# Performance work log

Measured on AMD Instinct MI355X. Metric: run time of the kernel, lower is better.

The kernel has to match this reference:

```python
import jax, jax.numpy as jnp
import numpy as np

B, N, C, H = 4, 1024, 1024, 16
HD = C // H


def setup_inputs() -> dict:
    key = jax.random.key(0)
    ks = jax.random.split(key, 9)
    s = 0.02
    return {
        "x": jax.random.normal(ks[0], (B, N, C), dtype=jnp.float32),
        "qkv_w": jax.random.normal(ks[1], (3 * C, C), dtype=jnp.float32) * s,
        "qkv_b": jax.random.normal(ks[2], (3 * C,), dtype=jnp.float32) * s,
        "proj_w": jax.random.normal(ks[3], (C, C), dtype=jnp.float32) * s,
        "proj_b": jax.random.normal(ks[4], (C,), dtype=jnp.float32) * s,
        "wl": jax.random.normal(ks[5], (H, H), dtype=jnp.float32) * s,
        "bl": jax.random.normal(ks[6], (H,), dtype=jnp.float32) * s,
        "ww": jax.random.normal(ks[7], (H, H), dtype=jnp.float32) * s,
        "bw": jax.random.normal(ks[8], (H,), dtype=jnp.float32) * s,
    }


def reference(x, qkv_w, qkv_b, proj_w, proj_b, wl, bl, ww, bw):
    # qkv: torch Linear convention y = x @ W.T + b
    scale = HD ** (-0.5)
    qkv = (jnp.einsum("bnc,oc->bno", x, qkv_w) + qkv_b)
    qkv = qkv.reshape(B, N, 3, H, HD).transpose(2, 0, 3, 1, 4)  # [3,B,H,N,HD]
    q, k, v = qkv[0] * scale, qkv[1], qkv[2]
    attn = jnp.einsum("bhnd,bhmd->bhnm", q, k)  # [B,H,N,N]
    # talking-heads mix before softmax (proj_l over head dim)
    attn = jnp.einsum("bhnm,gh->bgnm", attn, wl) + bl[:, None, None]
    attn = jax.nn.softmax(attn, axis=-1)
    # talking-heads mix after softmax (proj_w over head dim)
    attn = jnp.einsum("bhnm,gh->bgnm", attn, ww) + bw[:, None, None]
    out = jnp.einsum("bhnm,bhmd->bhnd", attn, v)  # [B,H,N,HD]
    out = out.transpose(0, 2, 1, 3).reshape(B, N, C)
    out = jnp.einsum("bnc,oc->bno", out, proj_w) + proj_b
    return out, attn
```

## Files before the change

kernel.cpp:

```cpp
#include <hip/hip_runtime.h>
#include <hip/hip_bf16.h>

typedef unsigned short u16;
typedef __attribute__((ext_vector_type(8))) __bf16 bf16x8;
typedef __attribute__((ext_vector_type(4))) float f32x4;

template <typename T> struct is16 { static constexpr bool v = false; };
template <> struct is16<u16> { static constexpr bool v = true; };

__device__ __forceinline__ float bf2f(u16 u) {
    unsigned int x = ((unsigned int)u) << 16;
    return __builtin_bit_cast(float, x);
}
__device__ __forceinline__ u16 f2bf(float f) {
    unsigned int x = __builtin_bit_cast(unsigned int, f);
    unsigned int lsb = (x >> 16) & 1u;
    x += 0x7fffu + lsb;
    return (u16)(x >> 16);
}

__device__ __forceinline__ void ld8(u16* dst, const u16* src) {
    *(float4*)dst = *(const float4*)src;
}
__device__ __forceinline__ void ld8(u16* dst, const float* src) {
    float4 a = *(const float4*)src;
    float4 b = *(const float4*)(src + 4);
    u16 t[8];
    t[0] = f2bf(a.x); t[1] = f2bf(a.y); t[2] = f2bf(a.z); t[3] = f2bf(a.w);
    t[4] = f2bf(b.x); t[5] = f2bf(b.y); t[6] = f2bf(b.z); t[7] = f2bf(b.w);
    *(float4*)dst = *(float4*)t;
}
__device__ __forceinline__ void stC(u16* p, float v)   { *p = f2bf(v); }
__device__ __forceinline__ void stC(float* p, float v) { *p = v; }

__device__ __forceinline__ void g2l16(const void* g, void* l) {
    __builtin_amdgcn_global_load_lds(
        (const __attribute__((address_space(1))) void*)g,
        (__attribute__((address_space(3))) void*)l, 16, 0, 0);
}

__global__ __launch_bounds__(256)
void cvt_bf16(const float* __restrict__ src, u16* __restrict__ dst)
{
    long long t = blockIdx.x * 256 + threadIdx.x;
    u16 tmp[8];
    ld8(tmp, src + t * 8);
    *(float4*)(dst + t * 8) = *(float4*)tmp;
}

template <typename TA, typename TB, typename TC>
__global__ __launch_bounds__(256)
void gemm_nt(const TA* __restrict__ A, long long sA, int lda,
             const TB* __restrict__ B, long long sB, int ldb,
             TC* __restrict__ C, long long sC, int ldc,
             const float* __restrict__ bias, int K)
{
    constexpr int SA = is16<TA>::v ? 32 : 40;
    constexpr int SB = is16<TB>::v ? 32 : 40;
    __shared__ u16 As[128 * SA];
    __shared__ u16 Bs[128 * SB];

    const int tid = threadIdx.x;
    const int z = blockIdx.z;
    A += (long long)z * sA;
    B += (long long)z * sB;
    C += (long long)z * sC;
    const int m0 = blockIdx.y * 128;
    const int n0 = blockIdx.x * 128;
    const int wid = tid >> 6;
    const int lane = tid & 63;
    const int wm = (wid >> 1) * 64;
    const int wn = (wid & 1) * 64;
    const int lr = lane & 15;
    const int quad = lane >> 4;

    f32x4 acc[4][4];
#pragma unroll
    for (int i = 0; i < 4; i++)
#pragma unroll
        for (int j = 0; j < 4; j++)
#pragma unroll
            for (int r = 0; r < 4; r++) acc[i][j][r] = 0.f;

    const int srow = tid >> 2;
    const int scol = (tid & 3) * 8;

    for (int k0 = 0; k0 < K; k0 += 32) {
        __syncthreads();
        const TA* ga = A + (long long)(m0 + srow) * lda + k0 + scol;
        if constexpr (is16<TA>::v) {
            g2l16(ga, (char*)As + tid * 16);
            g2l16(ga + (long long)64 * lda, (char*)As + 4096 + tid * 16);
        } else {
            ld8(&As[srow * SA + scol], ga);
            ld8(&As[(srow + 64) * SA + scol], ga + (long long)64 * lda);
        }
        const TB* gb = B + (long long)(n0 + srow) * ldb + k0 + scol;
        if constexpr (is16<TB>::v) {
            g2l16(gb, (char*)Bs + tid * 16);
            g2l16(gb + (long long)64 * ldb, (char*)Bs + 4096 + tid * 16);
        } else {
            ld8(&Bs[srow * SB + scol], gb);
            ld8(&Bs[(srow + 64) * SB + scol], gb + (long long)64 * ldb);
        }
        __syncthreads();

        bf16x8 af[4], bfr[4];
#pragma unroll
        for (int t = 0; t < 4; t++) {
            af[t]  = *(const bf16x8*)&As[(wm + t * 16 + lr) * SA + quad * 8];
            bfr[t] = *(const bf16x8*)&Bs[(wn + t * 16 + lr) * SB + quad * 8];
        }
#pragma unroll
        for (int i = 0; i < 4; i++)
#pragma unroll
            for (int j = 0; j < 4; j++)
                acc[i][j] = __builtin_amdgcn_mfma_f32_16x16x32_bf16(af[i], bfr[j], acc[i][j], 0, 0, 0);
    }

#pragma unroll
    for (int j = 0; j < 4; j++) {
        const int col = n0 + wn + j * 16 + lr;
        const float bv = bias ? bias[col] : 0.f;
#pragma unroll
        for (int i = 0; i < 4; i++) {
            const int rbase = m0 + wm + i * 16 + quad * 4;
#pragma unroll
            for (int r = 0; r < 4; r++)
                stC(&C[(long long)(rbase + r) * ldc + col], acc[i][j][r] + bv);
        }
    }
}

__global__ __launch_bounds__(256)
void reorder_qkv(const u16* __restrict__ y, u16* __restrict__ q,
                 u16* __restrict__ k, u16* __restrict__ v)
{
    int t = blockIdx.x * 256 + threadIdx.x;
    int which = t >> 19;
    int r = t & 524287;
    int d8 = r & 7;
    int n = (r >> 3) & 1023;
    int h = (r >> 13) & 15;
    int b = r >> 17;
    const u16* src = y + ((long long)(b * 1024 + n)) * 3072 + which * 1024 + h * 64 + d8 * 8;
    u16* dst = (which == 0 ? q : (which == 1 ? k : v)) +
               (((long long)((b * 16 + h) * 1024 + n)) * 64 + d8 * 8);
    float4 val = *(const float4*)src;
    if (which == 0) {
        u16 tmp[8];
        *(float4*)tmp = val;
#pragma unroll
        for (int i = 0; i < 8; i++) tmp[i] = f2bf(bf2f(tmp[i]) * 0.125f);
        val = *(float4*)tmp;
    }
    *(float4*)dst = val;
}

__global__ __launch_bounds__(256)
void mix_softmax(const u16* __restrict__ S, float* __restrict__ attn_out,
                 u16* __restrict__ attn_bf,
                 const float* __restrict__ wl, const float* __restrict__ bl,
                 const float* __restrict__ ww, const float* __restrict__ bw)
{
    __shared__ float wlT[256];
    __shared__ float wwS[256];
    __shared__ float blS[16];
    __shared__ float bwS[16];
    __shared__ float red[64];
    __shared__ float gsum[16];

    const int tid = threadIdx.x;
    const int lane = tid & 63;
    const int wid = tid >> 6;
    const int b = blockIdx.x >> 10, n = blockIdx.x & 1023;
    const int m0 = tid * 4;

    const long long base = ((long long)(b * 16) * 1024 + n) * 1024 + m0;

    ushort4 pre[4];
#pragma unroll
    for (int h = 0; h < 4; h++)
        pre[h] = *(const ushort4*)(S + base + (long long)h * 1048576);

    wlT[(tid & 15) * 16 + (tid >> 4)] = wl[tid];
    if (tid < 16) { blS[tid] = bl[tid]; bwS[tid] = bw[tid]; }
    __syncthreads();

    f32x4 a[16];
#pragma unroll
    for (int g = 0; g < 16; g++) {
        float bv = blS[g];
        a[g] = (f32x4){bv, bv, bv, bv};
    }

#pragma unroll
    for (int h = 0; h < 16; h++) {
        ushort4 r = pre[h & 3];
        if (h + 4 < 16)
            pre[h & 3] = *(const ushort4*)(S + base + (long long)(h + 4) * 1048576);
        f32x4 sv;
        sv.x = bf2f(r.x); sv.y = bf2f(r.y); sv.z = bf2f(r.z); sv.w = bf2f(r.w);
        float wr[16];
        *(f32x4*)&wr[0]  = *(const f32x4*)&wlT[h * 16];
        *(f32x4*)&wr[4]  = *(const f32x4*)&wlT[h * 16 + 4];
        *(f32x4*)&wr[8]  = *(const f32x4*)&wlT[h * 16 + 8];
        *(f32x4*)&wr[12] = *(const f32x4*)&wlT[h * 16 + 12];
#pragma unroll
        for (int g = 0; g < 16; g++)
            a[g] += sv * wr[g];
    }

#pragma unroll
    for (int g = 0; g < 16; g++) {
        f32x4 p;
        p.x = __expf(a[g].x);
        p.y = __expf(a[g].y);
        p.z = __expf(a[g].z);
        p.w = __expf(a[g].w);
        a[g] = p;
        float vv = (p.x + p.y) + (p.z + p.w);
        for (int off = 32; off; off >>= 1) vv += __shfl_xor(vv, off, 64);
        if (lane == 0) red[wid * 16 + g] = vv;
    }
    __syncthreads();
    if (tid < 16)
        gsum[tid] = (red[tid] + red[16 + tid]) + (red[32 + tid] + red[48 + tid]);
    __syncthreads();
    wwS[tid] = ww[tid] / gsum[tid & 15];
    __syncthreads();

#pragma unroll
    for (int g = 0; g < 16; g++) {
        float wr[16];
        *(f32x4*)&wr[0]  = *(const f32x4*)&wwS[g * 16];
        *(f32x4*)&wr[4]  = *(const f32x4*)&wwS[g * 16 + 4];
        *(f32x4*)&wr[8]  = *(const f32x4*)&wwS[g * 16 + 8];
        *(f32x4*)&wr[12] = *(const f32x4*)&wwS[g * 16 + 12];
        float bv = bwS[g];
        f32x4 o = (f32x4){bv, bv, bv, bv};
#pragma unroll
        for (int h = 0; h < 16; h++)
            o += a[h] * wr[h];
        const long long off = base + (long long)g * 1048576;
        __builtin_nontemporal_store(o, (f32x4*)(attn_out + off));
        ushort4 bo;
        bo.x = f2bf(o.x); bo.y = f2bf(o.y); bo.z = f2bf(o.z); bo.w = f2bf(o.w);
        *(ushort4*)(attn_bf + off) = bo;
    }
}

__global__ __launch_bounds__(256)
void av_gemm(const u16* __restrict__ attn_bf, const u16* __restrict__ v,
             u16* __restrict__ out1)
{
    __shared__ u16 As[64 * 32];
    __shared__ u16 Bs[64 * 40];

    const int tid = threadIdx.x;
    const int z = blockIdx.z;
    const int b = z >> 4, h = z & 15;
    const int m0 = blockIdx.x * 64;
    const u16* Ab = attn_bf + (long long)z * 1048576;
    const u16* Vb = v + (long long)z * 65536;
    const int wid = tid >> 6;
    const int lane = tid & 63;
    const int lr = lane & 15;
    const int quad = lane >> 4;
    const int wm = wid * 16;

    f32x4 acc[4];
#pragma unroll
    for (int j = 0; j < 4; j++)
#pragma unroll
        for (int r = 0; r < 4; r++) acc[j][r] = 0.f;

    const int srow = tid >> 2;
    const int scol = (tid & 3) * 8;
    const int vrow = tid >> 3;
    const int vdb = (tid & 7) * 8;

    for (int k0 = 0; k0 < 1024; k0 += 32) {
        __syncthreads();
        g2l16(Ab + (long long)(m0 + srow) * 1024 + k0 + scol, (char*)As + tid * 16);
        u16 tmp[8];
        *(float4*)tmp = *(const float4*)(Vb + (long long)(k0 + vrow) * 64 + vdb);
#pragma unroll
        for (int j = 0; j < 8; j++) Bs[(vdb + j) * 40 + vrow] = tmp[j];
        __syncthreads();

        bf16x8 af, bfr[4];
        af = *(const bf16x8*)&As[(wm + lr) * 32 + quad * 8];
#pragma unroll
        for (int t = 0; t < 4; t++)
            bfr[t] = *(const bf16x8*)&Bs[(t * 16 + lr) * 40 + quad * 8];
#pragma unroll
        for (int j = 0; j < 4; j++)
            acc[j] = __builtin_amdgcn_mfma_f32_16x16x32_bf16(af, bfr[j], acc[j], 0, 0, 0);
    }

#pragma unroll
    for (int j = 0; j < 4; j++) {
        const int col = h * 64 + j * 16 + lr;
        const int rbase = m0 + wm + quad * 4;
#pragma unroll
        for (int r = 0; r < 4; r++)
            out1[(long long)(b * 1024 + rbase + r) * 1024 + col] = f2bf(acc[j][r]);
    }
}

extern "C" void kernel_launch(void* const* d_in, const int* in_sizes, int n_in,
                              void* d_out, int out_size, void* d_ws, size_t ws_size,
                              hipStream_t stream)
{
    const float* x      = (const float*)d_in[0];
    const float* qkv_w  = (const float*)d_in[1];
    const float* qkv_b  = (const float*)d_in[2];
    const float* proj_w = (const float*)d_in[3];
    const float* proj_b = (const float*)d_in[4];
    const float* wl     = (const float*)d_in[5];
    const float* bl     = (const float*)d_in[6];
    const float* ww     = (const float*)d_in[7];
    const float* bw     = (const float*)d_in[8];

    float* out      = (float*)d_out;
    float* attn_out = out + 4194304;

    u16* ws   = (u16*)d_ws;
    u16* y    = ws;
    u16* q    = ws + 12582912;
    u16* k    = ws + 16777216;
    u16* v    = ws + 20971520;
    u16* s    = ws + 25165824;
    u16* out1 = ws;

    u16* xb  = s;
    u16* qwb = s + 4194304;
    u16* pwb = q;

    dim3 blk(256);
    cvt_bf16<<<dim3(2048), blk, 0, stream>>>(x, xb);
    cvt_bf16<<<dim3(1536), blk, 0, stream>>>(qkv_w, qwb);
    gemm_nt<u16, u16, u16><<<dim3(24, 32, 1), blk, 0, stream>>>(
        xb, 0, 1024, qwb, 0, 1024, y, 0, 3072, qkv_b, 1024);
    reorder_qkv<<<dim3(6144), blk, 0, stream>>>(y, q, k, v);
    gemm_nt<u16, u16, u16><<<dim3(8, 8, 64), blk, 0, stream>>>(
        q, 65536, 64, k, 65536, 64, s, 1048576, 1024, nullptr, 64);
    cvt_bf16<<<dim3(512), blk, 0, stream>>>(proj_w, pwb);
    mix_softmax<<<dim3(4096), blk, 0, stream>>>(s, attn_out, s, wl, bl, ww, bw);
    av_gemm<<<dim3(16, 1, 64), blk, 0, stream>>>(s, v, out1);
    gemm_nt<u16, u16, float><<<dim3(8, 32, 1), blk, 0, stream>>>(
        out1, 0, 1024, pwb, 0, 1024, out, 0, 1024, proj_b, 1024);
}
```

Baseline: 608.9 us.

## Remove QKV reorder kernel by strided GEMM reads and fuse bf16 conversions

```diff
diff --git a/kernel.cpp b/kernel.cpp
--- a/kernel.cpp
+++ b/kernel.cpp
@@ -40,20 +40,27 @@
 }
 
 __global__ __launch_bounds__(256)
-void cvt_bf16(const float* __restrict__ src, u16* __restrict__ dst)
-{
-    long long t = blockIdx.x * 256 + threadIdx.x;
+void cvt_all(const float* __restrict__ x, const float* __restrict__ qw,
+             const float* __restrict__ pw, u16* __restrict__ xb,
+             u16* __restrict__ qwb, u16* __restrict__ pwb)
+{
+    long long t = (long long)blockIdx.x * 256 + threadIdx.x;
+    const float* src; u16* dst; long long o;
+    if (t < 524288)      { src = x;  dst = xb;  o = t; }
+    else if (t < 917504) { src = qw; dst = qwb; o = t - 524288; }
+    else                 { src = pw; dst = pwb; o = t - 917504; }
     u16 tmp[8];
-    ld8(tmp, src + t * 8);
-    *(float4*)(dst + t * 8) = *(float4*)tmp;
+    ld8(tmp, src + o * 8);
+    *(float4*)(dst + o * 8) = *(float4*)tmp;
 }
 
 template <typename TA, typename TB, typename TC>
 __global__ __launch_bounds__(256)
-void gemm_nt(const TA* __restrict__ A, long long sA, int lda,
-             const TB* __restrict__ B, long long sB, int ldb,
-             TC* __restrict__ C, long long sC, int ldc,
-             const float* __restrict__ bias, int K)
+void gemm_nt(const TA* __restrict__ A, long long sAb, long long sAh, int lda,
+             const TB* __restrict__ B, long long sBb, long long sBh, int ldb,
+             TC* __restrict__ C, long long sCb, long long sCh, int ldc,
+             const float* __restrict__ bias, int K, int zdiv,
+             float cscale, int csplit)
 {
     constexpr int SA = is16<TA>::v ? 32 : 40;
     constexpr int SB = is16<TB>::v ? 32 : 40;
@@ -62,9 +69,10 @@
 
     const int tid = threadIdx.x;
     const int z = blockIdx.z;
-    A += (long long)z * sA;
-    B += (long long)z * sB;
-    C += (long long)z * sC;
+    const int zb = z / zdiv, zh = z % zdiv;
+    A += zb * sAb + zh * sAh;
+    B += zb * sBb + zh * sBh;
+    C += zb * sCb + zh * sCh;
     const int m0 = blockIdx.y * 128;
     const int n0 = blockIdx.x * 128;
     const int wid = tid >> 6;
@@ -122,39 +130,15 @@
     for (int j = 0; j < 4; j++) {
         const int col = n0 + wn + j * 16 + lr;
         const float bv = bias ? bias[col] : 0.f;
+        const float scl = (col < csplit) ? cscale : 1.f;
 #pragma unroll
         for (int i = 0; i < 4; i++) {
             const int rbase = m0 + wm + i * 16 + quad * 4;
 #pragma unroll
             for (int r = 0; r < 4; r++)
-                stC(&C[(long long)(rbase + r) * ldc + col], acc[i][j][r] + bv);
+                stC(&C[(long long)(rbase + r) * ldc + col], (acc[i][j][r] + bv) * scl);
         }
     }
-}
-
-__global__ __launch_bounds__(256)
-void reorder_qkv(const u16* __restrict__ y, u16* __restrict__ q,
-                 u16* __restrict__ k, u16* __restrict__ v)
-{
-    int t = blockIdx.x * 256 + threadIdx.x;
-    int which = t >> 19;
-    int r = t & 524287;
-    int d8 = r & 7;
-    int n = (r >> 3) & 1023;
-    int h = (r >> 13) & 15;
-    int b = r >> 17;
-    const u16* src = y + ((long long)(b * 1024 + n)) * 3072 + which * 1024 + h * 64 + d8 * 8;
-    u16* dst = (which == 0 ? q : (which == 1 ? k : v)) +
-               (((long long)((b * 16 + h) * 1024 + n)) * 64 + d8 * 8);
-    float4 val = *(const float4*)src;
-    if (which == 0) {
-        u16 tmp[8];
-        *(float4*)tmp = val;
-#pragma unroll
-        for (int i = 0; i < 8; i++) tmp[i] = f2bf(bf2f(tmp[i]) * 0.125f);
-        val = *(float4*)tmp;
-    }
-    *(float4*)dst = val;
 }
 
 __global__ __launch_bounds__(256)
@@ -178,9 +162,9 @@
 
     const long long base = ((long long)(b * 16) * 1024 + n) * 1024 + m0;
 
-    ushort4 pre[4];
-#pragma unroll
-    for (int h = 0; h < 4; h++)
+    ushort4 pre[8];
+#pragma unroll
+    for (int h = 0; h < 8; h++)
         pre[h] = *(const ushort4*)(S + base + (long long)h * 1048576);
 
     wlT[(tid & 15) * 16 + (tid >> 4)] = wl[tid];
@@ -196,9 +180,9 @@
 
 #pragma unroll
     for (int h = 0; h < 16; h++) {
-        ushort4 r = pre[h & 3];
-        if (h + 4 < 16)
-            pre[h & 3] = *(const ushort4*)(S + base + (long long)(h + 4) * 1048576);
+        ushort4 r = pre[h & 7];
+        if (h + 8 < 16)
+            pre[h & 7] = *(const ushort4*)(S + base + (long long)(h + 8) * 1048576);
         f32x4 sv;
         sv.x = bf2f(r.x); sv.y = bf2f(r.y); sv.z = bf2f(r.z); sv.w = bf2f(r.w);
         float wr[16];
@@ -251,7 +235,7 @@
 }
 
 __global__ __launch_bounds__(256)
-void av_gemm(const u16* __restrict__ attn_bf, const u16* __restrict__ v,
+void av_gemm(const u16* __restrict__ attn_bf, const u16* __restrict__ y,
              u16* __restrict__ out1)
 {
     __shared__ u16 As[64 * 32];
@@ -262,7 +246,7 @@
     const int b = z >> 4, h = z & 15;
     const int m0 = blockIdx.x * 64;
     const u16* Ab = attn_bf + (long long)z * 1048576;
-    const u16* Vb = v + (long long)z * 65536;
+    const u16* Vb = y + (long long)b * 3145728 + 2048 + h * 64;
     const int wid = tid >> 6;
     const int lane = tid & 63;
     const int lr = lane & 15;
@@ -284,7 +268,7 @@
         __syncthreads();
         g2l16(Ab + (long long)(m0 + srow) * 1024 + k0 + scol, (char*)As + tid * 16);
         u16 tmp[8];
-        *(float4*)tmp = *(const float4*)(Vb + (long long)(k0 + vrow) * 64 + vdb);
+        *(float4*)tmp = *(const float4*)(Vb + (long long)(k0 + vrow) * 3072 + vdb);
 #pragma unroll
         for (int j = 0; j < 8; j++) Bs[(vdb + j) * 40 + vrow] = tmp[j];
         __syncthreads();
@@ -328,27 +312,21 @@
 
     u16* ws   = (u16*)d_ws;
     u16* y    = ws;
-    u16* q    = ws + 12582912;
-    u16* k    = ws + 16777216;
-    u16* v    = ws + 20971520;
+    u16* out1 = ws + 12582912;
+    u16* pwb  = ws + 16777216;
     u16* s    = ws + 25165824;
-    u16* out1 = ws;
-
-    u16* xb  = s;
-    u16* qwb = s + 4194304;
-    u16* pwb = q;
+    u16* xb   = s;
+    u16* qwb  = s + 4194304;
 
     dim3 blk(256);
-    cvt_bf16<<<dim3(2048), blk, 0, stream>>>(x, xb);
-    cvt_bf16<<<dim3(1536), blk, 0, stream>>>(qkv_w, qwb);
+    cvt_all<<<dim3(4096), blk, 0, stream>>>(x, qkv_w, proj_w, xb, qwb, pwb);
     gemm_nt<u16, u16, u16><<<dim3(24, 32, 1), blk, 0, stream>>>(
-        xb, 0, 1024, qwb, 0, 1024, y, 0, 3072, qkv_b, 1024);
-    reorder_qkv<<<dim3(6144), blk, 0, stream>>>(y, q, k, v);
+        xb, 0, 0, 1024, qwb, 0, 0, 1024, y, 0, 0, 3072, qkv_b, 1024, 1, 0.125f, 1024);
     gemm_nt<u16, u16, u16><<<dim3(8, 8, 64), blk, 0, stream>>>(
-        q, 65536, 64, k, 65536, 64, s, 1048576, 1024, nullptr, 64);
-    cvt_bf16<<<dim3(512), blk, 0, stream>>>(proj_w, pwb);
+        y, 3145728, 64, 3072, y + 1024, 3145728, 64, 3072,
+        s, 16777216, 1048576, 1024, nullptr, 64, 16, 1.f, 0);
     mix_softmax<<<dim3(4096), blk, 0, stream>>>(s, attn_out, s, wl, bl, ww, bw);
-    av_gemm<<<dim3(16, 1, 64), blk, 0, stream>>>(s, v, out1);
+    av_gemm<<<dim3(16, 1, 64), blk, 0, stream>>>(s, y, out1);
     gemm_nt<u16, u16, float><<<dim3(8, 32, 1), blk, 0, stream>>>(
-        out1, 0, 1024, pwb, 0, 1024, out, 0, 1024, proj_b, 1024);
-}
+        out1, 0, 0, 1024, pwb, 0, 0, 1024, out, 0, 0, 1024, proj_b, 1024, 1, 1.f, 0);
+}
```

Result: faster. 596.1 us (-2.1%).
